# Optimization experiments

Measured on AMD Instinct MI355X. Metric: run time of the kernel, lower is better.

## Reference

```python
import jax, jax.numpy as jnp
import numpy as np

TOP_K = 2  # num_experts_per_tok


def setup_inputs() -> dict:
    key = jax.random.key(0)
    ks = jax.random.split(key, 4)
    B, S, H, I, E = 4, 2048, 2048, 4096, 8
    std = 0.02
    hidden_states = jax.random.normal(ks[0], (B, S, H), dtype=jnp.float32)
    gate_w = jax.random.normal(ks[1], (E, H), dtype=jnp.float32) * std   # nn.Linear weight [E,H]
    wfc = jax.random.normal(ks[2], (E, I, H), dtype=jnp.float32) * std   # c_fc weight [E,out,in]
    bfc = jnp.zeros((E, I), dtype=jnp.float32)                           # bias zero-init
    wproj = jax.random.normal(ks[3], (E, H, I), dtype=jnp.float32) * std # c_proj weight
    bproj = jnp.zeros((E, H), dtype=jnp.float32)
    return {"hidden_states": hidden_states, "gate_w": gate_w, "wfc": wfc,
            "bfc": bfc, "wproj": wproj, "bproj": bproj}


def reference(hidden_states, gate_w, wfc, bfc, wproj, bproj):
    B, S, H = hidden_states.shape
    E = wfc.shape[0]
    x = hidden_states.reshape(-1, H)                      # [T, H]
    router_logits = x @ gate_w.T                          # [T, E]
    top_vals, top_idx = jax.lax.top_k(router_logits, TOP_K)
    router_weights = jax.nn.softmax(top_vals.astype(jnp.float32), axis=-1).astype(x.dtype)  # [T, k]
    out = jnp.zeros_like(x)
    # Loop over the small fixed set of experts; each token contributes with its
    # combined gate weight for that expert (0 if not routed there). Same math as
    # the torch gather/grouped-GEMM/scatter-add path.
    for e in range(E):
        gate_e = jnp.sum(jnp.where(top_idx == e, router_weights, 0.0), axis=-1)  # [T]
        h = jax.nn.gelu(x @ wfc[e].T + bfc[e], approximate=False)                # [T, I]
        y = h @ wproj[e].T + bproj[e]                                            # [T, H]
        out = out + gate_e[:, None] * y
    return out.reshape(B, S, H), router_logits
```

## Files before the change

### kernel.cpp

```cpp
#include <hip/hip_runtime.h>
#include <hip/hip_bf16.h>
#include <math.h>

#define NT 8192
#define HD 2048
#define ID 4096
#define NE 8
#define MAXSLOT 18432
#define MAXRB 72

typedef __bf16 bf16x8 __attribute__((ext_vector_type(8)));
typedef float f32x4 __attribute__((ext_vector_type(4)));

__device__ __forceinline__ float bf2f(unsigned short u){
  union{unsigned u; float f;} v; v.u = ((unsigned)u) << 16; return v.f;
}

__device__ __forceinline__ void gload_lds16(const void* g, void* l){
  __builtin_amdgcn_global_load_lds((const __attribute__((address_space(1))) void*)g,
                                   (__attribute__((address_space(3))) void*)l, 16, 0, 0);
}

__global__ __launch_bounds__(256) void cvt_kernel(const float* __restrict__ in,
                                                  __hip_bfloat16* __restrict__ outp, int n4){
  int i = blockIdx.x * blockDim.x + threadIdx.x;
  int stride = gridDim.x * blockDim.x;
  for (; i < n4; i += stride){
    float4 v = reinterpret_cast<const float4*>(in)[i];
    union{ushort4 u; __hip_bfloat16 h[4];} o;
    o.h[0] = __float2bfloat16(v.x); o.h[1] = __float2bfloat16(v.y);
    o.h[2] = __float2bfloat16(v.z); o.h[3] = __float2bfloat16(v.w);
    reinterpret_cast<ushort4*>(outp)[i] = o.u;
  }
}

__global__ __launch_bounds__(256) void gather_cvt_kernel(
    const float* __restrict__ x, const int* __restrict__ slotTok,
    __hip_bfloat16* __restrict__ xg)
{
  const int slot = blockIdx.x;
  const int c = threadIdx.x * 8;
  const int pr = slotTok[slot];
  ushort4* dst = reinterpret_cast<ushort4*>(xg + (long)slot * HD + c);
  if (pr < 0){
    ushort4 z = {0,0,0,0};
    dst[0] = z; dst[1] = z;
    return;
  }
  const float* src = x + (long)(pr >> 1) * HD + c;
  float4 v0 = reinterpret_cast<const float4*>(src)[0];
  float4 v1 = reinterpret_cast<const float4*>(src)[1];
  union{ushort4 u; __hip_bfloat16 h[4];} a, b;
  a.h[0]=__float2bfloat16(v0.x); a.h[1]=__float2bfloat16(v0.y);
  a.h[2]=__float2bfloat16(v0.z); a.h[3]=__float2bfloat16(v0.w);
  b.h[0]=__float2bfloat16(v1.x); b.h[1]=__float2bfloat16(v1.y);
  b.h[2]=__float2bfloat16(v1.z); b.h[3]=__float2bfloat16(v1.w);
  dst[0] = a.u; dst[1] = b.u;
}

__global__ __launch_bounds__(256) void router_kernel(
    const float* __restrict__ x, const float* __restrict__ gw,
    float* __restrict__ logits_out, int* __restrict__ tokExp,
    float* __restrict__ tokW, int* __restrict__ cnt)
{
  int wave = (blockIdx.x * blockDim.x + threadIdx.x) >> 6;
  int lane = threadIdx.x & 63;
  if (wave >= NT) return;
  const float* xr = x + (long)wave * HD;
  double acc[NE];
  #pragma unroll
  for (int e = 0; e < NE; e++) acc[e] = 0.0;
  for (int k = lane; k < HD; k += 64){
    double xv = (double)xr[k];
    #pragma unroll
    for (int e = 0; e < NE; e++) acc[e] += xv * (double)gw[e * HD + k];
  }
  #pragma unroll
  for (int e = 0; e < NE; e++){
    #pragma unroll
    for (int off = 32; off; off >>= 1) acc[e] += __shfl_down(acc[e], off, 64);
  }
  if (lane == 0){
    int e0 = 0; double v0 = acc[0];
    for (int e = 1; e < NE; e++) if (acc[e] > v0){ v0 = acc[e]; e0 = e; }
    int e1 = -1; double v1 = -1e300;
    for (int e = 0; e < NE; e++) if (e != e0 && acc[e] > v1){ v1 = acc[e]; e1 = e; }
    double ex = exp(v1 - v0);
    double s = 1.0 + ex;
    for (int e = 0; e < NE; e++) logits_out[wave * NE + e] = (float)acc[e];
    tokExp[wave * 2]     = e0; tokExp[wave * 2 + 1] = e1;
    tokW[wave * 2]       = (float)(1.0 / s);
    tokW[wave * 2 + 1]   = (float)(ex / s);
    atomicAdd(&cnt[e0], 1); atomicAdd(&cnt[e1], 1);
  }
}

__global__ void offsets_kernel(const int* __restrict__ cnt, int* __restrict__ padOff){
  if (threadIdx.x == 0 && blockIdx.x == 0){
    int o = 0;
    for (int e = 0; e < NE; e++){ padOff[e] = o; o += ((cnt[e] + 255) >> 8) << 8; }
    padOff[NE] = o;
  }
}

__global__ __launch_bounds__(256) void scatter_kernel(
    const int* __restrict__ tokExp, const int* __restrict__ padOff, int* cursor,
    int* __restrict__ slotTok)
{
  int t = blockIdx.x * blockDim.x + threadIdx.x;
  if (t >= NT) return;
  #pragma unroll
  for (int s = 0; s < 2; s++){
    int e = tokExp[t * 2 + s];
    int pos = atomicAdd(&cursor[e], 1);
    slotTok[padOff[e] + pos] = t * 2 + s;
  }
}


#define LDA(buf,kk,m) (*reinterpret_cast<const bf16x8*>(&lds[((buf)*2+(kk))*8192 + (wr*8+(m))*512 + laneF]))
#define LDB(buf,kk,n) (*reinterpret_cast<const bf16x8*>(&lds[32768 + ((buf)*2+(kk))*8192 + (wc*4+(n))*512 + laneF]))
#define STAGE_A(buf,kk,koff) do{ \
    __hip_bfloat16* d_ = &lds[((buf)*2+(kk))*8192 + w*1024]; \
    gload_lds16(aS0 + (koff), d_); \
    gload_lds16(aS1 + (koff), d_ + 512); \
  }while(0)
#define STAGE_B(buf,kk,koff) do{ \
    __hip_bfloat16* d_ = &lds[32768 + ((buf)*2+(kk))*8192 + w*1024]; \
    gload_lds16(bS0 + (koff), d_); \
    gload_lds16(bS1 + (koff), d_ + 512); \
  }while(0)
#define MFMA16(M0,A0_,A1_,A2_,A3_) do{ \
    acc[(M0)+0][0] = __builtin_amdgcn_mfma_f32_16x16x32_bf16(A0_, bv0, acc[(M0)+0][0],0,0,0); \
    acc[(M0)+1][0] = __builtin_amdgcn_mfma_f32_16x16x32_bf16(A1_, bv0, acc[(M0)+1][0],0,0,0); \
    acc[(M0)+2][0] = __builtin_amdgcn_mfma_f32_16x16x32_bf16(A2_, bv0, acc[(M0)+2][0],0,0,0); \
    acc[(M0)+3][0] = __builtin_amdgcn_mfma_f32_16x16x32_bf16(A3_, bv0, acc[(M0)+3][0],0,0,0); \
    acc[(M0)+0][1] = __builtin_amdgcn_mfma_f32_16x16x32_bf16(A0_, bv1, acc[(M0)+0][1],0,0,0); \
    acc[(M0)+1][1] = __builtin_amdgcn_mfma_f32_16x16x32_bf16(A1_, bv1, acc[(M0)+1][1],0,0,0); \
    acc[(M0)+2][1] = __builtin_amdgcn_mfma_f32_16x16x32_bf16(A2_, bv1, acc[(M0)+2][1],0,0,0); \
    acc[(M0)+3][1] = __builtin_amdgcn_mfma_f32_16x16x32_bf16(A3_, bv1, acc[(M0)+3][1],0,0,0); \
    acc[(M0)+0][2] = __builtin_amdgcn_mfma_f32_16x16x32_bf16(A0_, bv2, acc[(M0)+0][2],0,0,0); \
    acc[(M0)+1][2] = __builtin_amdgcn_mfma_f32_16x16x32_bf16(A1_, bv2, acc[(M0)+1][2],0,0,0); \
    acc[(M0)+2][2] = __builtin_amdgcn_mfma_f32_16x16x32_bf16(A2_, bv2, acc[(M0)+2][2],0,0,0); \
    acc[(M0)+3][2] = __builtin_amdgcn_mfma_f32_16x16x32_bf16(A3_, bv2, acc[(M0)+3][2],0,0,0); \
    acc[(M0)+0][3] = __builtin_amdgcn_mfma_f32_16x16x32_bf16(A0_, bv3, acc[(M0)+0][3],0,0,0); \
    acc[(M0)+1][3] = __builtin_amdgcn_mfma_f32_16x16x32_bf16(A1_, bv3, acc[(M0)+1][3],0,0,0); \
    acc[(M0)+2][3] = __builtin_amdgcn_mfma_f32_16x16x32_bf16(A2_, bv3, acc[(M0)+2][3],0,0,0); \
    acc[(M0)+3][3] = __builtin_amdgcn_mfma_f32_16x16x32_bf16(A3_, bv3, acc[(M0)+3][3],0,0,0); \
  }while(0)

template<int AGATHER, int WSC, int EPI, int ND, int KD>
__global__ __launch_bounds__(512, 2) void moe_gemm8(
    const __hip_bfloat16* __restrict__ A,
    const __hip_bfloat16* __restrict__ W,
    const float* __restrict__ bias,
    const int* __restrict__ slotTok,
    const int* __restrict__ padOff,
    __hip_bfloat16* __restrict__ Yout)
{
  __shared__ __align__(16) __hip_bfloat16 lds[65536];
  const int bid = blockIdx.x;
  const int xcd = bid & 7;
  const int g   = bid >> 3;
  const int cb  = xcd + 8 * (g / MAXRB);
  const int rb  = g % MAXRB;
  if (rb * 256 >= padOff[NE]) return;
  int e = 0;
  #pragma unroll
  for (int i = 1; i < NE; i++) if (rb * 256 >= padOff[i]) e = i;

  const int tid  = threadIdx.x;
  const int lane = tid & 63;
  const int w    = tid >> 6;
  const int wr   = w >> 2;
  const int wc   = w & 3;

  const int r16s = lane >> 2;
  const int cgs  = (lane & 3) ^ ((r16s >> 1) & 3);
  const int r0 = rb * 256 + 32 * w + r16s;
  long ga0, ga1;
  if (AGATHER == 0){
    ga0 = r0; ga1 = r0 + 16;
  } else {
    int p0 = slotTok[r0], p1 = slotTok[r0 + 16];
    ga0 = p0 < 0 ? 0 : (AGATHER == 1 ? (p0 >> 1) : p0);
    ga1 = p1 < 0 ? 0 : (AGATHER == 1 ? (p1 >> 1) : p1);
  }
  const __hip_bfloat16* aS0 = A + ga0 * (long)KD + cgs * 8;
  const __hip_bfloat16* aS1 = A + ga1 * (long)KD + cgs * 8;
  const long rowB = (long)cb * 256 + 32 * w + r16s;
  const __hip_bfloat16* bS0 = W + (long)e * ND * KD + rowB * KD + cgs * 8;
  const __hip_bfloat16* bS1 = bS0 + 16 * (long)KD;

  const int r16f = lane & 15;
  const int chf  = lane >> 4;
  const int laneF = r16f * 32 + (chf ^ ((r16f >> 1) & 3)) * 8;

  f32x4 acc[8][4] = {};
  bf16x8 bv0, bv1, bv2, bv3;

  constexpr int NTILES = KD / 64;

  STAGE_A(0,0,0);   STAGE_B(0,0,0);
  STAGE_A(0,1,32);  STAGE_B(0,1,32);
  STAGE_A(1,0,64);  STAGE_B(1,0,64);
  STAGE_A(1,1,96);  STAGE_B(1,1,96);
  asm volatile("s_waitcnt vmcnt(8)" ::: "memory");
  __builtin_amdgcn_s_barrier();

  for (int t = 0; t < NTILES; ++t){
    const int b = t & 1;
    const bool s01 = (t >= 1) && (t + 1 < NTILES);
    const bool s23 = (t + 2 < NTILES);
    const long ko01 = (long)(t + 1) * 64 + 32;
    const long ko23 = (long)(t + 2) * 64;
    {
      bf16x8 a0 = LDA(b,0,0), a1 = LDA(b,0,1), a2 = LDA(b,0,2), a3 = LDA(b,0,3);
      bv0 = LDB(b,0,0); bv1 = LDB(b,0,1); bv2 = LDB(b,0,2); bv3 = LDB(b,0,3);
      if (s01){ STAGE_A(b^1,1,ko01); }
      __builtin_amdgcn_s_barrier();
      asm volatile("s_waitcnt lgkmcnt(0)" ::: "memory");
      __builtin_amdgcn_s_setprio(1);
      MFMA16(0, a0, a1, a2, a3);
      __builtin_amdgcn_s_setprio(0);
      __builtin_amdgcn_s_barrier();
    }
    {
      bf16x8 a0 = LDA(b,0,4), a1 = LDA(b,0,5), a2 = LDA(b,0,6), a3 = LDA(b,0,7);
      if (s01){ STAGE_B(b^1,1,ko01); }
      __builtin_amdgcn_s_barrier();
      asm volatile("s_waitcnt lgkmcnt(0)" ::: "memory");
      __builtin_amdgcn_s_setprio(1);
      MFMA16(4, a0, a1, a2, a3);
      __builtin_amdgcn_s_setprio(0);
      __builtin_amdgcn_s_barrier();
    }
    {
      bf16x8 a0 = LDA(b,1,0), a1 = LDA(b,1,1), a2 = LDA(b,1,2), a3 = LDA(b,1,3);
      bv0 = LDB(b,1,0); bv1 = LDB(b,1,1); bv2 = LDB(b,1,2); bv3 = LDB(b,1,3);
      if (s23){ STAGE_A(b,0,ko23); }
      __builtin_amdgcn_s_barrier();
      asm volatile("s_waitcnt lgkmcnt(0)" ::: "memory");
      __builtin_amdgcn_s_setprio(1);
      MFMA16(0, a0, a1, a2, a3);
      __builtin_amdgcn_s_setprio(0);
      __builtin_amdgcn_s_barrier();
    }
    {
      bf16x8 a0 = LDA(b,1,4), a1 = LDA(b,1,5), a2 = LDA(b,1,6), a3 = LDA(b,1,7);
      if (s23){ STAGE_B(b,0,ko23); }
      __builtin_amdgcn_s_barrier();
      asm volatile("s_waitcnt lgkmcnt(0)" ::: "memory");
      __builtin_amdgcn_s_setprio(1);
      MFMA16(4, a0, a1, a2, a3);
      __builtin_amdgcn_s_setprio(0);
      if (s23) asm volatile("s_waitcnt vmcnt(4)" ::: "memory");
      else     asm volatile("s_waitcnt vmcnt(0)" ::: "memory");
      __builtin_amdgcn_s_barrier();
    }
  }

  const int colBase = cb * 256 + wc * 64 + (lane & 15);
  const int rowQ = (lane >> 4) * 4;
  float bb[4];
  #pragma unroll
  for (int n = 0; n < 4; n++) bb[n] = bias[(long)e * ND + colBase + n * 16];
  #pragma unroll
  for (int m = 0; m < 8; m++){
    const int grow = rb * 256 + wr * 128 + m * 16 + rowQ;
    #pragma unroll
    for (int r = 0; r < 4; r++){
      long orow;
      bool doW;
      if (WSC == 0){ orow = grow + r; doW = true; }
      else { int pr = slotTok[grow + r]; orow = pr; doW = (pr >= 0); }
      if (doW){
        #pragma unroll
        for (int n = 0; n < 4; n++){
          float v = acc[m][n][r] + bb[n];
          if (EPI == 0){
            v = 0.5f * v * (1.0f + erff(v * 0.70710678118654752f));
          }
          Yout[orow * ND + colBase + n * 16] = __float2bfloat16(v);
        }
      }
    }
  }
}

__global__ __launch_bounds__(256) void combine_kernel(
    const __hip_bfloat16* __restrict__ yb, const float* __restrict__ tokW,
    float* __restrict__ outp)
{
  const int t  = blockIdx.x;
  const int c0 = threadIdx.x * 8;
  const float w0 = tokW[t * 2], w1 = tokW[t * 2 + 1];
  const ushort4* p0 = reinterpret_cast<const ushort4*>(yb + (long)(2 * t) * HD + c0);
  const ushort4* p1 = reinterpret_cast<const ushort4*>(yb + (long)(2 * t + 1) * HD + c0);
  float4 o[2];
  #pragma unroll
  for (int h = 0; h < 2; h++){
    ushort4 a = p0[h], b = p1[h];
    o[h].x = w0 * bf2f(a.x) + w1 * bf2f(b.x);
    o[h].y = w0 * bf2f(a.y) + w1 * bf2f(b.y);
    o[h].z = w0 * bf2f(a.z) + w1 * bf2f(b.z);
    o[h].w = w0 * bf2f(a.w) + w1 * bf2f(b.w);
  }
  __syncthreads();
  float4* po = reinterpret_cast<float4*>(outp + (long)t * HD + c0);
  po[0] = o[0]; po[1] = o[1];
}

extern "C" void kernel_launch(void* const* d_in, const int* in_sizes, int n_in,
                              void* d_out, int out_size, void* d_ws, size_t ws_size,
                              hipStream_t stream)
{
  (void)in_sizes; (void)n_in; (void)out_size;
  const float* x     = (const float*)d_in[0];
  const float* gw    = (const float*)d_in[1];
  const float* wfc   = (const float*)d_in[2];
  const float* bfc   = (const float*)d_in[3];
  const float* wproj = (const float*)d_in[4];
  const float* bproj = (const float*)d_in[5];
  float* outp   = (float*)d_out;
  float* logits = outp + (size_t)NT * HD;
  __hip_bfloat16* yb = (__hip_bfloat16*)d_out;

  char* ws = (char*)d_ws;
  size_t off = 0;
  auto alloc = [&](size_t b){ void* p = ws + off; off += (b + 255) & ~(size_t)255; return p; };

  const size_t XG_B  = (size_t)MAXSLOT * HD * 2;
  const size_t HBS_B = (size_t)MAXSLOT * ID * 2;
  const size_t WB_B  = (size_t)NE * ID * HD * 2;
  const size_t MISC_B = (size_t)MAXSLOT*4 + NT*2*4 + NT*2*4 + 4096;
  const bool slotPath = (XG_B + HBS_B + WB_B + MISC_B + 4096) <= ws_size;

  __hip_bfloat16 *xg, *hb, *wB;
  if (slotPath){
    xg = (__hip_bfloat16*)alloc(XG_B);
    hb = (__hip_bfloat16*)alloc(HBS_B);
    wB = (__hip_bfloat16*)alloc(WB_B);
  } else {
    xg = (__hip_bfloat16*)alloc((size_t)NT * HD * 2);
    hb = (__hip_bfloat16*)alloc((size_t)NT * 2 * ID * 2);
    wB = (__hip_bfloat16*)alloc(WB_B);
  }
  int*   slotTok = (int*)alloc(MAXSLOT * 4);
  int*   tokExp  = (int*)alloc(NT * 2 * 4);
  float* tokW    = (float*)alloc(NT * 2 * 4);
  int*   meta    = (int*)alloc(256);
  int* cnt = meta; int* cursor = meta + 8; int* padOff = meta + 16;

  hipMemsetAsync(meta, 0, 256, stream);
  hipMemsetAsync(slotTok, 0xFF, MAXSLOT * 4, stream);

  router_kernel<<<NT / 4, 256, 0, stream>>>(x, gw, logits, tokExp, tokW, cnt);
  offsets_kernel<<<1, 64, 0, stream>>>(cnt, padOff);
  scatter_kernel<<<NT / 256, 256, 0, stream>>>(tokExp, padOff, cursor, slotTok);

  if (slotPath){
    gather_cvt_kernel<<<MAXSLOT, 256, 0, stream>>>(x, slotTok, xg);
    cvt_kernel<<<2048, 256, 0, stream>>>(wfc, wB, NE * ID * HD / 4);
    moe_gemm8<0, 0, 0, ID, HD><<<(ID / 256) * MAXRB, 512, 0, stream>>>(xg, wB, bfc, slotTok, padOff, hb);
    cvt_kernel<<<2048, 256, 0, stream>>>(wproj, wB, NE * HD * ID / 4);
    moe_gemm8<0, 1, 1, HD, ID><<<(HD / 256) * MAXRB, 512, 0, stream>>>(hb, wB, bproj, slotTok, padOff, yb);
  } else {
    cvt_kernel<<<2048, 256, 0, stream>>>(x, xg, NT * HD / 4);
    cvt_kernel<<<2048, 256, 0, stream>>>(wfc, wB, NE * ID * HD / 4);
    moe_gemm8<1, 1, 0, ID, HD><<<(ID / 256) * MAXRB, 512, 0, stream>>>(xg, wB, bfc, slotTok, padOff, hb);
    cvt_kernel<<<2048, 256, 0, stream>>>(wproj, wB, NE * HD * ID / 4);
    moe_gemm8<2, 1, 1, HD, ID><<<(HD / 256) * MAXRB, 512, 0, stream>>>(hb, wB, bproj, slotTok, padOff, yb);
  }

  combine_kernel<<<NT, 256, 0, stream>>>(yb, tokW, outp);
}
```

Before: 1.249 ms.

## Restructure MoE GEMM K-loop into 4-slot ring buffer with 3-stage prefetch

Replaces the double-buffered 64-wide K tile pipeline (four sub-phases, staggered A/B staging) with a four-slot ring of 32-wide K stages, each holding A and B together, prefetched three stages ahead. Each iteration now has two compute phases and issues one combined stage load, with vmcnt waits adjusted by remaining stages. The aim is deeper memory prefetch and fewer barriers per MFMA. The trade-off is more loop iterations, each doing half the work, and different barrier and wait placement that must stay correct across slot reuse.

```diff
diff --git a/kernel.cpp b/kernel.cpp
--- a/kernel.cpp
+++ b/kernel.cpp
@@ -118,17 +118,15 @@
 }
 
 
-#define LDA(buf,kk,m) (*reinterpret_cast<const bf16x8*>(&lds[((buf)*2+(kk))*8192 + (wr*8+(m))*512 + laneF]))
-#define LDB(buf,kk,n) (*reinterpret_cast<const bf16x8*>(&lds[32768 + ((buf)*2+(kk))*8192 + (wc*4+(n))*512 + laneF]))
-#define STAGE_A(buf,kk,koff) do{ \
-    __hip_bfloat16* d_ = &lds[((buf)*2+(kk))*8192 + w*1024]; \
-    gload_lds16(aS0 + (koff), d_); \
-    gload_lds16(aS1 + (koff), d_ + 512); \
-  }while(0)
-#define STAGE_B(buf,kk,koff) do{ \
-    __hip_bfloat16* d_ = &lds[32768 + ((buf)*2+(kk))*8192 + w*1024]; \
-    gload_lds16(bS0 + (koff), d_); \
-    gload_lds16(bS1 + (koff), d_ + 512); \
+#define LDA(sb,m) (*reinterpret_cast<const bf16x8*>(&lds[(sb) + (wr*8+(m))*512 + laneF]))
+#define LDB(sb,n) (*reinterpret_cast<const bf16x8*>(&lds[(sb) + 8192 + (wc*4+(n))*512 + laneF]))
+#define STAGE(s,koff) do{ \
+    __hip_bfloat16* dA_ = &lds[((s)&3)*16384 + w*1024]; \
+    gload_lds16(aS0 + (koff), dA_); \
+    gload_lds16(aS1 + (koff), dA_ + 512); \
+    __hip_bfloat16* dB_ = dA_ + 8192; \
+    gload_lds16(bS0 + (koff), dB_); \
+    gload_lds16(bS1 + (koff), dB_ + 512); \
   }while(0)
 #define MFMA16(M0,A0_,A1_,A2_,A3_) do{ \
     acc[(M0)+0][0] = __builtin_amdgcn_mfma_f32_16x16x32_bf16(A0_, bv0, acc[(M0)+0][0],0,0,0); \
@@ -150,7 +148,7 @@
   }while(0)
 
 template<int AGATHER, int WSC, int EPI, int ND, int KD>
-__global__ __launch_bounds__(512, 2) void moe_gemm8(
+__global__ __launch_bounds__(512, 2) void moe_gemm12(
     const __hip_bfloat16* __restrict__ A,
     const __hip_bfloat16* __restrict__ W,
     const float* __restrict__ bias,
@@ -199,25 +197,20 @@
   f32x4 acc[8][4] = {};
   bf16x8 bv0, bv1, bv2, bv3;
 
-  constexpr int NTILES = KD / 64;
-
-  STAGE_A(0,0,0);   STAGE_B(0,0,0);
-  STAGE_A(0,1,32);  STAGE_B(0,1,32);
-  STAGE_A(1,0,64);  STAGE_B(1,0,64);
-  STAGE_A(1,1,96);  STAGE_B(1,1,96);
+  constexpr int NS = KD / 32;
+
+  STAGE(0, 0);
+  STAGE(1, 32);
+  STAGE(2, 64);
   asm volatile("s_waitcnt vmcnt(8)" ::: "memory");
   __builtin_amdgcn_s_barrier();
 
-  for (int t = 0; t < NTILES; ++t){
-    const int b = t & 1;
-    const bool s01 = (t >= 1) && (t + 1 < NTILES);
-    const bool s23 = (t + 2 < NTILES);
-    const long ko01 = (long)(t + 1) * 64 + 32;
-    const long ko23 = (long)(t + 2) * 64;
+  for (int t = 0; t < NS; ++t){
+    const int sb = (t & 3) * 16384;
     {
-      bf16x8 a0 = LDA(b,0,0), a1 = LDA(b,0,1), a2 = LDA(b,0,2), a3 = LDA(b,0,3);
-      bv0 = LDB(b,0,0); bv1 = LDB(b,0,1); bv2 = LDB(b,0,2); bv3 = LDB(b,0,3);
-      if (s01){ STAGE_A(b^1,1,ko01); }
+      bf16x8 a0 = LDA(sb,0), a1 = LDA(sb,1), a2 = LDA(sb,2), a3 = LDA(sb,3);
+      bv0 = LDB(sb,0); bv1 = LDB(sb,1); bv2 = LDB(sb,2); bv3 = LDB(sb,3);
+      if (t + 3 < NS){ STAGE(t + 3, (long)(t + 3) * 32); }
       __builtin_amdgcn_s_barrier();
       asm volatile("s_waitcnt lgkmcnt(0)" ::: "memory");
       __builtin_amdgcn_s_setprio(1);
@@ -226,36 +219,16 @@
       __builtin_amdgcn_s_barrier();
     }
     {
-      bf16x8 a0 = LDA(b,0,4), a1 = LDA(b,0,5), a2 = LDA(b,0,6), a3 = LDA(b,0,7);
-      if (s01){ STAGE_B(b^1,1,ko01); }
+      bf16x8 a0 = LDA(sb,4), a1 = LDA(sb,5), a2 = LDA(sb,6), a3 = LDA(sb,7);
       __builtin_amdgcn_s_barrier();
       asm volatile("s_waitcnt lgkmcnt(0)" ::: "memory");
       __builtin_amdgcn_s_setprio(1);
       MFMA16(4, a0, a1, a2, a3);
       __builtin_amdgcn_s_setprio(0);
-      __builtin_amdgcn_s_barrier();
-    }
-    {
-      bf16x8 a0 = LDA(b,1,0), a1 = LDA(b,1,1), a2 = LDA(b,1,2), a3 = LDA(b,1,3);
-      bv0 = LDB(b,1,0); bv1 = LDB(b,1,1); bv2 = LDB(b,1,2); bv3 = LDB(b,1,3);
-      if (s23){ STAGE_A(b,0,ko23); }
-      __builtin_amdgcn_s_barrier();
-      asm volatile("s_waitcnt lgkmcnt(0)" ::: "memory");
-      __builtin_amdgcn_s_setprio(1);
-      MFMA16(0, a0, a1, a2, a3);
-      __builtin_amdgcn_s_setprio(0);
-      __builtin_amdgcn_s_barrier();
-    }
-    {
-      bf16x8 a0 = LDA(b,1,4), a1 = LDA(b,1,5), a2 = LDA(b,1,6), a3 = LDA(b,1,7);
-      if (s23){ STAGE_B(b,0,ko23); }
-      __builtin_amdgcn_s_barrier();
-      asm volatile("s_waitcnt lgkmcnt(0)" ::: "memory");
-      __builtin_amdgcn_s_setprio(1);
-      MFMA16(4, a0, a1, a2, a3);
-      __builtin_amdgcn_s_setprio(0);
-      if (s23) asm volatile("s_waitcnt vmcnt(4)" ::: "memory");
-      else     asm volatile("s_waitcnt vmcnt(0)" ::: "memory");
+      const int rem = NS - 1 - t;
+      if (rem >= 3)      asm volatile("s_waitcnt vmcnt(8)" ::: "memory");
+      else if (rem == 2) asm volatile("s_waitcnt vmcnt(4)" ::: "memory");
+      else if (rem == 1) asm volatile("s_waitcnt vmcnt(0)" ::: "memory");
       __builtin_amdgcn_s_barrier();
     }
   }
@@ -362,15 +335,15 @@
   if (slotPath){
     gather_cvt_kernel<<<MAXSLOT, 256, 0, stream>>>(x, slotTok, xg);
     cvt_kernel<<<2048, 256, 0, stream>>>(wfc, wB, NE * ID * HD / 4);
-    moe_gemm8<0, 0, 0, ID, HD><<<(ID / 256) * MAXRB, 512, 0, stream>>>(xg, wB, bfc, slotTok, padOff, hb);
+    moe_gemm12<0, 0, 0, ID, HD><<<(ID / 256) * MAXRB, 512, 0, stream>>>(xg, wB, bfc, slotTok, padOff, hb);
     cvt_kernel<<<2048, 256, 0, stream>>>(wproj, wB, NE * HD * ID / 4);
-    moe_gemm8<0, 1, 1, HD, ID><<<(HD / 256) * MAXRB, 512, 0, stream>>>(hb, wB, bproj, slotTok, padOff, yb);
+    moe_gemm12<0, 1, 1, HD, ID><<<(HD / 256) * MAXRB, 512, 0, stream>>>(hb, wB, bproj, slotTok, padOff, yb);
   } else {
     cvt_kernel<<<2048, 256, 0, stream>>>(x, xg, NT * HD / 4);
     cvt_kernel<<<2048, 256, 0, stream>>>(wfc, wB, NE * ID * HD / 4);
-    moe_gemm8<1, 1, 0, ID, HD><<<(ID / 256) * MAXRB, 512, 0, stream>>>(xg, wB, bfc, slotTok, padOff, hb);
+    moe_gemm12<1, 1, 0, ID, HD><<<(ID / 256) * MAXRB, 512, 0, stream>>>(xg, wB, bfc, slotTok, padOff, hb);
     cvt_kernel<<<2048, 256, 0, stream>>>(wproj, wB, NE * HD * ID / 4);
-    moe_gemm8<2, 1, 1, HD, ID><<<(HD / 256) * MAXRB, 512, 0, stream>>>(hb, wB, bproj, slotTok, padOff, yb);
+    moe_gemm12<2, 1, 1, HD, ID><<<(HD / 256) * MAXRB, 512, 0, stream>>>(hb, wB, bproj, slotTok, padOff, yb);
   }
 
   combine_kernel<<<NT, 256, 0, stream>>>(yb, tokW, outp);
```

After: 1.298 ms. 3.9% more time.
